# Performance work log

Hardware: AMD Instinct MI355X
Metric: run time of the kernel (lower is better)

## Reference

```python
import jax, jax.numpy as jnp
import numpy as np

B, S, H = 2, 1024, 2048
E, I, K = 32, 768, 4


def setup_inputs() -> dict:
    key = jax.random.key(0)
    k1, k2, k3, k4, k5 = jax.random.split(key, 5)
    sH = 1.0 / np.sqrt(H)
    sI = 1.0 / np.sqrt(I)
    return {
        "hidden_states": jax.random.normal(k1, (B, S, H), dtype=jnp.float32),
        "gate_w": jax.random.normal(k2, (E, H), dtype=jnp.float32) * sH,
        "w_gate": jax.random.normal(k3, (E, H, I), dtype=jnp.float32) * sH,
        "w_up": jax.random.normal(k4, (E, H, I), dtype=jnp.float32) * sH,
        "w_down": jax.random.normal(k5, (E, I, H), dtype=jnp.float32) * sI,
        "top_k": K,
    }


def reference(hidden_states, gate_w, w_gate, w_up, w_down, top_k):
    b, s, h = hidden_states.shape
    x = hidden_states.reshape(-1, h)                      # [T, H]
    T = x.shape[0]

    # Router: logits -> softmax over experts -> top-k -> renormalize
    logits = x @ gate_w.T                                 # [T, E]
    probs = jax.nn.softmax(logits, axis=-1)
    topv, topi = jax.lax.top_k(probs, top_k)              # [T, K]
    topv = topv / jnp.sum(topv, axis=-1, keepdims=True)   # norm_topk_prob

    # Dense routing-weight matrix (zero except selected experts) [T, E]
    rw = jnp.zeros((T, probs.shape[-1]), dtype=x.dtype)
    rw = rw.at[jnp.arange(T)[:, None], topi].set(topv)

    # Expert SwiGLU MLPs, computed for all experts then masked-combined
    g = jnp.einsum('th,ehi->eti', x, w_gate)              # [E, T, I]
    u = jnp.einsum('th,ehi->eti', x, w_up)                # [E, T, I]
    act = jax.nn.silu(g) * u                              # [E, T, I]
    expert_out = jnp.einsum('eti,eih->eth', act, w_down)  # [E, T, H]

    out = jnp.einsum('te,eth->th', rw, expert_out)        # combine [T, H]
    return out.reshape(b, s, h).astype(hidden_states.dtype)
```

## Files before the change

### kernel.cpp

```cpp
#include <hip/hip_runtime.h>
#include <hip/hip_bf16.h>
#include <math.h>

typedef unsigned short u16;
typedef unsigned int u32;
typedef unsigned long long u64;
typedef short s16x8 __attribute__((ext_vector_type(8)));
typedef u16 u16x8 __attribute__((ext_vector_type(8)));
typedef u32 u32x2 __attribute__((ext_vector_type(2)));
typedef u32 u32x4 __attribute__((ext_vector_type(4)));
typedef float f32x4 __attribute__((ext_vector_type(4)));

#define TTOK 2048
#define HDIM 2048
#define ENUM 32
#define IDIM 768
#define KTOP 4

#define WS_XB   0L
#define WS_ACT  8388608L
#define WS_TIDX 20971520L
#define WS_TW   (WS_TIDX + 32768L)
#define WS_CNT  (WS_TW + 32768L)
#define WS_OFFS (WS_CNT + 128L)
#define WS_CUR  (WS_OFFS + 256L)
#define WS_RTOK (WS_CUR + 128L)
#define WS_RW   (WS_RTOK + 32768L)
#define WS_RMAP (WS_RW + 32768L)
#define WS_EO   25165824L
#define WS_NEED (WS_EO + 33554432L)

#define LDBW 20

__device__ __forceinline__ u16 f2bf(float f) {
  unsigned u = __builtin_bit_cast(unsigned, f);
  unsigned r = (u + 0x7fffu + ((u >> 16) & 1u)) >> 16;
  return (u16)r;
}

__device__ __forceinline__ u32 cvtpk(float lo, float hi) {
  u32 r;
  asm("v_cvt_pk_bf16_f32 %0, %1, %2" : "=v"(r) : "v"(lo), "v"(hi));
  return r;
}

__device__ __forceinline__ void gll16(const void* g, void* l) {
  u32 loff = __builtin_amdgcn_readfirstlane((u32)(u64)l);
  __builtin_amdgcn_global_load_lds(
      (const __attribute__((address_space(1))) u32*)(u64)g,
      (__attribute__((address_space(3))) u32*)loff, 16, 0, 0);
}

__device__ __forceinline__ s16x8 bfrag(const u32* B, int d0, int d1) {
  u32x2 lo = *(const u32x2*)(B + d0);
  u32x2 hi = *(const u32x2*)(B + d1);
  u32x4 v = {lo.x, lo.y, hi.x, hi.y};
  return __builtin_bit_cast(s16x8, v);
}

__global__ __launch_bounds__(256) void router_kernel(const float* __restrict__ x,
                                                     const float* __restrict__ gw,
                                                     u16* __restrict__ xb,
                                                     int* __restrict__ tidx,
                                                     float* __restrict__ tw,
                                                     int* __restrict__ counts) {
  __shared__ float xs[HDIM];
  __shared__ float part[256];
  __shared__ float lg[ENUM];
  int t = blockIdx.x;
  const float4* xr = (const float4*)(x + (long)t * HDIM);
  float4* xs4 = (float4*)xs;
  for (int i = threadIdx.x; i < HDIM / 4; i += 256) xs4[i] = xr[i];
  __syncthreads();
  {
    int i0 = threadIdx.x * 8;
    uint4 o;
    o.x = cvtpk(xs[i0], xs[i0 + 1]);
    o.y = cvtpk(xs[i0 + 2], xs[i0 + 3]);
    o.z = cvtpk(xs[i0 + 4], xs[i0 + 5]);
    o.w = cvtpk(xs[i0 + 6], xs[i0 + 7]);
    *(uint4*)(xb + (long)t * HDIM + i0) = o;
  }
  int e = threadIdx.x >> 3, ch = threadIdx.x & 7;
  const float4* gp = (const float4*)(gw + (long)e * HDIM + ch * 256);
  const float4* xp = (const float4*)(xs + ch * 256);
  float s = 0.f;
#pragma unroll 8
  for (int c = 0; c < 64; c++) {
    float4 gv = gp[c], xv = xp[c];
    s += gv.x * xv.x + gv.y * xv.y + gv.z * xv.z + gv.w * xv.w;
  }
  part[threadIdx.x] = s;
  __syncthreads();
  if (threadIdx.x < 32) {
    float v = 0.f;
#pragma unroll
    for (int j = 0; j < 8; j++) v += part[threadIdx.x * 8 + j];
    lg[threadIdx.x] = v;
  }
  __syncthreads();
  if (threadIdx.x == 0) {
    int sel[KTOP]; float sv[KTOP];
    unsigned mask = 0;
    for (int k = 0; k < KTOP; k++) {
      float best = -INFINITY; int bi = 0;
      for (int j = 0; j < ENUM; j++)
        if (!((mask >> j) & 1u) && lg[j] > best) { best = lg[j]; bi = j; }
      mask |= 1u << bi; sel[k] = bi; sv[k] = best;
    }
    float m = sv[0], den = 0.f, ex[KTOP];
    for (int k = 0; k < KTOP; k++) { ex[k] = expf(sv[k] - m); den += ex[k]; }
    for (int k = 0; k < KTOP; k++) {
      tidx[t * KTOP + k] = sel[k];
      tw[t * KTOP + k] = ex[k] / den;
      atomicAdd(&counts[sel[k]], 1);
    }
  }
}

__global__ void scan_kernel(const int* __restrict__ counts, int* __restrict__ offs,
                            int* __restrict__ cur) {
  if (threadIdx.x == 0) {
    int a = 0;
    for (int e = 0; e < ENUM; e++) { offs[e] = a; a += counts[e]; }
    offs[ENUM] = a;
  }
  if (threadIdx.x < ENUM) cur[threadIdx.x] = 0;
}

__global__ __launch_bounds__(256) void scatter_kernel(const int* __restrict__ tidx,
                                                      const float* __restrict__ tw,
                                                      const int* __restrict__ offs,
                                                      int* __restrict__ cur,
                                                      int* __restrict__ rtok,
                                                      float* __restrict__ rw,
                                                      int* __restrict__ rowmap) {
  int i = blockIdx.x * 256 + threadIdx.x;
  int e = tidx[i];
  int pos = atomicAdd(&cur[e], 1);
  int row = offs[e] + pos;
  rtok[row] = i >> 2;
  rw[row] = tw[i];
  rowmap[i] = row;
}

__global__ __launch_bounds__(512) void gemm1_kernel(const u16* __restrict__ xb,
                                                    const float* __restrict__ wgp,
                                                    const float* __restrict__ wup,
                                                    const int* __restrict__ offs,
                                                    const int* __restrict__ rtok,
                                                    u16* __restrict__ act) {
  int d = blockIdx.x;
  int g = d % 384;
  int mt = d / 384;
  int e = g / 12;
  int nt = g % 12;
  int off = offs[e], cnt = offs[e + 1] - off;
  int m0 = mt << 8;
  if (m0 >= cnt) return;
  int rows = cnt - m0; if (rows > 256) rows = 256;
  int baser = off + m0;
  int n0 = nt << 6;

  __shared__ __align__(16) u16 As[2][256 * 32];
  __shared__ __align__(16) u32 Bs[2][2][64 * LDBW];

  int tid = threadIdx.x;
  int ln = tid & 63, w = tid >> 6;
  int wm = w >> 1, wn = w & 1;
  int lhi = ln >> 4, llo = ln & 15;

  const u16* gA[2];
  int ldsA[2];
#pragma unroll
  for (int j = 0; j < 2; j++) {
    int idx = w * 2 + j;
    int r = idx * 16 + (ln >> 2);
    int c = ln & 3;
    int csrc = c ^ ((r >> 1) & 3);
    int rr = r < rows ? r : rows - 1;
    gA[j] = xb + (long)rtok[baser + rr] * HDIM + csrc * 8;
    ldsA[j] = idx * 1024;
  }

  int mat = tid >> 8;
  int t2 = tid & 255;
  int a = t2 & 15;
  int kk = t2 >> 4;
  const float* gB = (mat ? wup : wgp) + (long)e * ((long)HDIM * IDIM) +
                    (long)(2 * kk) * IDIM + n0 + 4 * a;
  int fB = 2 * (a & 7);
  int wOff[4];
#pragma unroll
  for (int j = 0; j < 4; j++) wOff[j] = (4 * a + j) * LDBW + (kk ^ fB);

  int offA[4];
#pragma unroll
  for (int mf = 0; mf < 4; mf++) {
    int r = wm * 64 + mf * 16 + llo;
    offA[mf] = r * 64 + ((lhi ^ ((r >> 1) & 3)) * 16);
  }
  int dB0[2], dB1[2];
#pragma unroll
  for (int nf = 0; nf < 2; nf++) {
    int n = wn * 32 + nf * 16 + llo;
    int f = 2 * ((n >> 2) & 7);
    dB0[nf] = n * LDBW + ((4 * lhi) ^ f);
    dB1[nf] = n * LDBW + (((4 * lhi) | 2) ^ f);
  }

  f32x4 accg[4][2], accu[4][2];
  f32x4 zz = {0.f, 0.f, 0.f, 0.f};
#pragma unroll
  for (int i = 0; i < 4; i++)
#pragma unroll
    for (int j = 0; j < 2; j++) { accg[i][j] = zz; accu[i][j] = zz; }

  float4 rB0, rB1;

  rB0 = *(const float4*)gB;
  rB1 = *(const float4*)(gB + IDIM);
  gll16(gA[0], (char*)As[0] + ldsA[0]);
  gll16(gA[1], (char*)As[0] + ldsA[1]);
  {
    u32* bb = &Bs[0][mat][0];
    bb[wOff[0]] = cvtpk(rB0.x, rB1.x);
    bb[wOff[1]] = cvtpk(rB0.y, rB1.y);
    bb[wOff[2]] = cvtpk(rB0.z, rB1.z);
    bb[wOff[3]] = cvtpk(rB0.w, rB1.w);
  }
  __syncthreads();

  const int NS = HDIM / 32;
  int buf = 0;
  for (int t = 0; t < NS; ++t) {
    if (t + 1 < NS) {
      const float* p = gB + (long)(t + 1) * 32 * IDIM;
      rB0 = *(const float4*)p;
      rB1 = *(const float4*)(p + IDIM);
      gll16(gA[0] + (t + 1) * 32, (char*)As[buf ^ 1] + ldsA[0]);
      gll16(gA[1] + (t + 1) * 32, (char*)As[buf ^ 1] + ldsA[1]);
    }
    __builtin_amdgcn_sched_barrier(0);
    {
      const char* Ab = (const char*)As[buf];
      const u32* Bg = &Bs[buf][0][0];
      const u32* Bu = &Bs[buf][1][0];
      s16x8 av[4];
#pragma unroll
      for (int mf = 0; mf < 4; mf++) av[mf] = *(const s16x8*)(Ab + offA[mf]);
#pragma unroll
      for (int nf = 0; nf < 2; nf++) {
        s16x8 bg = bfrag(Bg, dB0[nf], dB1[nf]);
        s16x8 bu = bfrag(Bu, dB0[nf], dB1[nf]);
#pragma unroll
        for (int mf = 0; mf < 4; mf++) {
          accg[mf][nf] = __builtin_amdgcn_mfma_f32_16x16x32_bf16(av[mf], bg, accg[mf][nf], 0, 0, 0);
          accu[mf][nf] = __builtin_amdgcn_mfma_f32_16x16x32_bf16(av[mf], bu, accu[mf][nf], 0, 0, 0);
        }
      }
    }
    if (t + 1 < NS) {
      u32* bb = &Bs[buf ^ 1][mat][0];
      bb[wOff[0]] = cvtpk(rB0.x, rB1.x);
      bb[wOff[1]] = cvtpk(rB0.y, rB1.y);
      bb[wOff[2]] = cvtpk(rB0.z, rB1.z);
      bb[wOff[3]] = cvtpk(rB0.w, rB1.w);
    }
    __syncthreads();
    buf ^= 1;
  }

  int rb = wm * 64 + lhi * 4;
  int cb = n0 + wn * 32 + llo;
#pragma unroll
  for (int mf = 0; mf < 4; mf++) {
#pragma unroll
    for (int r4 = 0; r4 < 4; r4++) {
      int rl = rb + mf * 16 + r4;
      if (rl < rows) {
        long rowb = (long)(baser + rl) * IDIM;
#pragma unroll
        for (int nf = 0; nf < 2; nf++) {
          float g2 = accg[mf][nf][r4], u = accu[mf][nf][r4];
          float av = g2 / (1.f + __expf(-g2)) * u;
          act[rowb + cb + nf * 16] = f2bf(av);
        }
      }
    }
  }
}

template <int STORE>
__global__ __launch_bounds__(512) void gemm2_kernel(const u16* __restrict__ act,
                                                    const float* __restrict__ wdp,
                                                    const int* __restrict__ offs,
                                                    const int* __restrict__ rtok,
                                                    const float* __restrict__ rw,
                                                    u16* __restrict__ eo,
                                                    float* __restrict__ out) {
  int d = blockIdx.x;
  int g = d & 511;
  int mt = d >> 9;
  int e = g >> 4;
  int nt = g & 15;
  int off = offs[e], cnt = offs[e + 1] - off;
  int m0 = mt << 8;
  if (m0 >= cnt) return;
  int rows = cnt - m0; if (rows > 256) rows = 256;
  int baser = off + m0;
  int n0 = nt << 7;

  __shared__ __align__(16) u16 As[2][256 * 32];
  __shared__ __align__(16) u32 Bs[2][128 * LDBW];

  int tid = threadIdx.x;
  int ln = tid & 63, w = tid >> 6;
  int wm = w >> 1, wn = w & 1;
  int lhi = ln >> 4, llo = ln & 15;

  const u16* gA[2];
  int ldsA[2];
#pragma unroll
  for (int j = 0; j < 2; j++) {
    int idx = w * 2 + j;
    int r = idx * 16 + (ln >> 2);
    int c = ln & 3;
    int csrc = c ^ ((r >> 1) & 3);
    int rr = r < rows ? r : rows - 1;
    gA[j] = act + (long)(baser + rr) * IDIM + csrc * 8;
    ldsA[j] = idx * 1024;
  }

  int a = tid & 31;
  int kk = (tid >> 5) & 15;
  const float* gB = wdp + (long)e * ((long)IDIM * HDIM) +
                    (long)(2 * kk) * HDIM + n0 + 4 * a;
  int fB = 2 * (a & 7);
  int wOff[4];
#pragma unroll
  for (int j = 0; j < 4; j++) wOff[j] = (4 * a + j) * LDBW + (kk ^ fB);

  int offA[4];
#pragma unroll
  for (int mf = 0; mf < 4; mf++) {
    int r = wm * 64 + mf * 16 + llo;
    offA[mf] = r * 64 + ((lhi ^ ((r >> 1) & 3)) * 16);
  }
  int dB0[4], dB1[4];
#pragma unroll
  for (int nf = 0; nf < 4; nf++) {
    int n = wn * 64 + nf * 16 + llo;
    int f = 2 * ((n >> 2) & 7);
    dB0[nf] = n * LDBW + ((4 * lhi) ^ f);
    dB1[nf] = n * LDBW + (((4 * lhi) | 2) ^ f);
  }

  f32x4 acc[4][4];
  f32x4 zz = {0.f, 0.f, 0.f, 0.f};
#pragma unroll
  for (int i = 0; i < 4; i++)
#pragma unroll
    for (int j = 0; j < 4; j++) acc[i][j] = zz;

  float4 rB0, rB1;

  rB0 = *(const float4*)gB;
  rB1 = *(const float4*)(gB + HDIM);
  gll16(gA[0], (char*)As[0] + ldsA[0]);
  gll16(gA[1], (char*)As[0] + ldsA[1]);
  {
    u32* bb = &Bs[0][0];
    bb[wOff[0]] = cvtpk(rB0.x, rB1.x);
    bb[wOff[1]] = cvtpk(rB0.y, rB1.y);
    bb[wOff[2]] = cvtpk(rB0.z, rB1.z);
    bb[wOff[3]] = cvtpk(rB0.w, rB1.w);
  }
  __syncthreads();

  const int NS = IDIM / 32;
  int buf = 0;
  for (int t = 0; t < NS; ++t) {
    if (t + 1 < NS) {
      const float* p = gB + (long)(t + 1) * 32 * HDIM;
      rB0 = *(const float4*)p;
      rB1 = *(const float4*)(p + HDIM);
      gll16(gA[0] + (t + 1) * 32, (char*)As[buf ^ 1] + ldsA[0]);
      gll16(gA[1] + (t + 1) * 32, (char*)As[buf ^ 1] + ldsA[1]);
    }
    __builtin_amdgcn_sched_barrier(0);
    {
      const char* Ab = (const char*)As[buf];
      const u32* Bb = &Bs[buf][0];
      s16x8 av[4];
#pragma unroll
      for (int mf = 0; mf < 4; mf++) av[mf] = *(const s16x8*)(Ab + offA[mf]);
#pragma unroll
      for (int nf = 0; nf < 4; nf++) {
        s16x8 bv = bfrag(Bb, dB0[nf], dB1[nf]);
#pragma unroll
        for (int mf = 0; mf < 4; mf++)
          acc[mf][nf] = __builtin_amdgcn_mfma_f32_16x16x32_bf16(av[mf], bv, acc[mf][nf], 0, 0, 0);
      }
    }
    if (t + 1 < NS) {
      u32* bb = &Bs[buf ^ 1][0];
      bb[wOff[0]] = cvtpk(rB0.x, rB1.x);
      bb[wOff[1]] = cvtpk(rB0.y, rB1.y);
      bb[wOff[2]] = cvtpk(rB0.z, rB1.z);
      bb[wOff[3]] = cvtpk(rB0.w, rB1.w);
    }
    __syncthreads();
    buf ^= 1;
  }

  int rb = wm * 64 + lhi * 4;
  int cb = n0 + wn * 64 + llo;
#pragma unroll
  for (int mf = 0; mf < 4; mf++) {
#pragma unroll
    for (int r4 = 0; r4 < 4; r4++) {
      int rl = rb + mf * 16 + r4;
      if (rl < rows) {
        int rr = baser + rl;
        if (STORE) {
          long ob = (long)rr * HDIM + cb;
#pragma unroll
          for (int nf = 0; nf < 4; nf++)
            eo[ob + nf * 16] = f2bf(acc[mf][nf][r4]);
        } else {
          float wt = rw[rr];
          long ob = (long)rtok[rr] * HDIM + cb;
#pragma unroll
          for (int nf = 0; nf < 4; nf++)
            atomicAdd(&out[ob + nf * 16], acc[mf][nf][r4] * wt);
        }
      }
    }
  }
}

__global__ __launch_bounds__(256) void combine_kernel(const u16* __restrict__ eo,
                                                      const int* __restrict__ rowmap,
                                                      const float* __restrict__ tw,
                                                      float* __restrict__ out) {
  int t = blockIdx.x;
  int h0 = threadIdx.x * 8;
  float acc[8] = {0.f, 0.f, 0.f, 0.f, 0.f, 0.f, 0.f, 0.f};
#pragma unroll
  for (int k = 0; k < KTOP; k++) {
    int r = rowmap[t * KTOP + k];
    float wt = tw[t * KTOP + k];
    u16x8 v = *(const u16x8*)(eo + (long)r * HDIM + h0);
#pragma unroll
    for (int j = 0; j < 8; j++)
      acc[j] += wt * __builtin_bit_cast(float, ((u32)v[j]) << 16);
  }
  float4 o0 = {acc[0], acc[1], acc[2], acc[3]};
  float4 o1 = {acc[4], acc[5], acc[6], acc[7]};
  *(float4*)(out + (long)t * HDIM + h0) = o0;
  *(float4*)(out + (long)t * HDIM + h0 + 4) = o1;
}

extern "C" void kernel_launch(void* const* d_in, const int* in_sizes, int n_in,
                              void* d_out, int out_size, void* d_ws, size_t ws_size,
                              hipStream_t stream) {
  const float* x = (const float*)d_in[0];
  const float* gw = (const float*)d_in[1];
  const float* wgate = (const float*)d_in[2];
  const float* wup = (const float*)d_in[3];
  const float* wdown = (const float*)d_in[4];
  float* out = (float*)d_out;

  char* ws = (char*)d_ws;
  u16* xb = (u16*)(ws + WS_XB);
  u16* act = (u16*)(ws + WS_ACT);
  int* tidx = (int*)(ws + WS_TIDX);
  float* tw = (float*)(ws + WS_TW);
  int* cnt = (int*)(ws + WS_CNT);
  int* offs = (int*)(ws + WS_OFFS);
  int* cur = (int*)(ws + WS_CUR);
  int* rtok = (int*)(ws + WS_RTOK);
  float* rw = (float*)(ws + WS_RW);
  int* rowmap = (int*)(ws + WS_RMAP);
  u16* eo = (u16*)(ws + WS_EO);
  bool storeMode = (ws_size >= (size_t)WS_NEED);

  hipMemsetAsync(cnt, 0, 128, stream);
  if (!storeMode)
    hipMemsetAsync(d_out, 0, (size_t)out_size * sizeof(float), stream);

  hipLaunchKernelGGL(router_kernel, dim3(TTOK), dim3(256), 0, stream, x, gw, xb, tidx, tw, cnt);
  hipLaunchKernelGGL(scan_kernel, dim3(1), dim3(64), 0, stream, cnt, offs, cur);
  hipLaunchKernelGGL(scatter_kernel, dim3(TTOK * KTOP / 256), dim3(256), 0, stream, tidx, tw, offs, cur, rtok, rw, rowmap);
  hipLaunchKernelGGL(gemm1_kernel, dim3(32 * 12 * 8), dim3(512), 0, stream, xb, wgate, wup, offs, rtok, act);
  if (storeMode) {
    hipLaunchKernelGGL(gemm2_kernel<1>, dim3(32 * 16 * 8), dim3(512), 0, stream, act, wdown, offs, rtok, rw, eo, out);
    hipLaunchKernelGGL(combine_kernel, dim3(TTOK), dim3(256), 0, stream, eo, rowmap, tw, out);
  } else {
    hipLaunchKernelGGL(gemm2_kernel<0>, dim3(32 * 16 * 8), dim3(512), 0, stream, act, wdown, offs, rtok, rw, eo, out);
  }
}
```

Baseline: 370.2 us.

## Split gate/up GEMM into separate tiles and add a SwiGLU fuse kernel

In store mode the fused gate+up GEMM is replaced by a kernel where each block computes only one of the two matrices for its tile. This doubles the grid and halves the B-tile shared memory per block. Gate and up results go to bf16 scratch buffers, and a separate elementwise kernel applies SiLU(g)*u to build the activation. The aim is more parallelism and occupancy, at the cost of reading A twice, extra global traffic for the intermediates, an extra launch, and bf16 rounding of g and u before the activation.

```diff
diff --git a/kernel.cpp b/kernel.cpp
--- a/kernel.cpp
+++ b/kernel.cpp
@@ -28,6 +28,8 @@
 #define WS_RW   (WS_RTOK + 32768L)
 #define WS_RMAP (WS_RW + 32768L)
 #define WS_EO   25165824L
+#define WS_GBUF WS_EO
+#define WS_UBUF (WS_EO + 12582912L)
 #define WS_NEED (WS_EO + 33554432L)
 
 #define LDBW 20
@@ -144,12 +146,175 @@
   rowmap[i] = row;
 }
 
-__global__ __launch_bounds__(512) void gemm1_kernel(const u16* __restrict__ xb,
-                                                    const float* __restrict__ wgp,
-                                                    const float* __restrict__ wup,
-                                                    const int* __restrict__ offs,
-                                                    const int* __restrict__ rtok,
-                                                    u16* __restrict__ act) {
+__global__ __launch_bounds__(512) void gemm1s_kernel(const u16* __restrict__ xb,
+                                                     const float* __restrict__ wgp,
+                                                     const float* __restrict__ wup,
+                                                     const int* __restrict__ offs,
+                                                     const int* __restrict__ rtok,
+                                                     u16* __restrict__ gbuf,
+                                                     u16* __restrict__ ubuf) {
+  int d = blockIdx.x;
+  int g = d % 768;
+  int mt = d / 768;
+  int e = g / 24;
+  int r24 = g % 24;
+  int nt = r24 >> 1;
+  int mat = r24 & 1;
+  int off = offs[e], cnt = offs[e + 1] - off;
+  int m0 = mt << 8;
+  if (m0 >= cnt) return;
+  int rows = cnt - m0; if (rows > 256) rows = 256;
+  int baser = off + m0;
+  int n0 = nt << 6;
+
+  __shared__ __align__(16) u16 As[2][256 * 32];
+  __shared__ __align__(16) u32 Bs[2][64 * LDBW];
+
+  int tid = threadIdx.x;
+  int ln = tid & 63, w = tid >> 6;
+  int wm = w >> 1, wn = w & 1;
+  int lhi = ln >> 4, llo = ln & 15;
+
+  const u16* gA[2];
+  int ldsA[2];
+#pragma unroll
+  for (int j = 0; j < 2; j++) {
+    int idx = w * 2 + j;
+    int r = idx * 16 + (ln >> 2);
+    int c = ln & 3;
+    int csrc = c ^ ((r >> 1) & 3);
+    int rr = r < rows ? r : rows - 1;
+    gA[j] = xb + (long)rtok[baser + rr] * HDIM + csrc * 8;
+    ldsA[j] = idx * 1024;
+  }
+
+  int isB = (tid < 256);
+  int a = tid & 15;
+  int kk = (tid >> 4) & 15;
+  const float* gB = (mat ? wup : wgp) + (long)e * ((long)HDIM * IDIM) +
+                    (long)(2 * kk) * IDIM + n0 + 4 * a;
+  int fB = 2 * (a & 7);
+  int wOff[4];
+#pragma unroll
+  for (int j = 0; j < 4; j++) wOff[j] = (4 * a + j) * LDBW + (kk ^ fB);
+
+  int offA[4];
+#pragma unroll
+  for (int mf = 0; mf < 4; mf++) {
+    int r = wm * 64 + mf * 16 + llo;
+    offA[mf] = r * 64 + ((lhi ^ ((r >> 1) & 3)) * 16);
+  }
+  int dB0[2], dB1[2];
+#pragma unroll
+  for (int nf = 0; nf < 2; nf++) {
+    int n = wn * 32 + nf * 16 + llo;
+    int f = 2 * ((n >> 2) & 7);
+    dB0[nf] = n * LDBW + ((4 * lhi) ^ f);
+    dB1[nf] = n * LDBW + (((4 * lhi) | 2) ^ f);
+  }
+
+  f32x4 acc[4][2];
+  f32x4 zz = {0.f, 0.f, 0.f, 0.f};
+#pragma unroll
+  for (int i = 0; i < 4; i++)
+#pragma unroll
+    for (int j = 0; j < 2; j++) acc[i][j] = zz;
+
+  float4 rB0, rB1;
+
+  if (isB) {
+    rB0 = *(const float4*)gB;
+    rB1 = *(const float4*)(gB + IDIM);
+  }
+  gll16(gA[0], (char*)As[0] + ldsA[0]);
+  gll16(gA[1], (char*)As[0] + ldsA[1]);
+  if (isB) {
+    u32* bb = &Bs[0][0];
+    bb[wOff[0]] = cvtpk(rB0.x, rB1.x);
+    bb[wOff[1]] = cvtpk(rB0.y, rB1.y);
+    bb[wOff[2]] = cvtpk(rB0.z, rB1.z);
+    bb[wOff[3]] = cvtpk(rB0.w, rB1.w);
+  }
+  __syncthreads();
+
+  const int NS = HDIM / 32;
+  int buf = 0;
+  for (int t = 0; t < NS; ++t) {
+    if (t + 1 < NS) {
+      if (isB) {
+        const float* p = gB + (long)(t + 1) * 32 * IDIM;
+        rB0 = *(const float4*)p;
+        rB1 = *(const float4*)(p + IDIM);
+      }
+      gll16(gA[0] + (t + 1) * 32, (char*)As[buf ^ 1] + ldsA[0]);
+      gll16(gA[1] + (t + 1) * 32, (char*)As[buf ^ 1] + ldsA[1]);
+    }
+    __builtin_amdgcn_sched_barrier(0);
+    {
+      const char* Ab = (const char*)As[buf];
+      const u32* Bb = &Bs[buf][0];
+      s16x8 av[4];
+#pragma unroll
+      for (int mf = 0; mf < 4; mf++) av[mf] = *(const s16x8*)(Ab + offA[mf]);
+#pragma unroll
+      for (int nf = 0; nf < 2; nf++) {
+        s16x8 bv = bfrag(Bb, dB0[nf], dB1[nf]);
+#pragma unroll
+        for (int mf = 0; mf < 4; mf++)
+          acc[mf][nf] = __builtin_amdgcn_mfma_f32_16x16x32_bf16(av[mf], bv, acc[mf][nf], 0, 0, 0);
+      }
+    }
+    if (t + 1 < NS && isB) {
+      u32* bb = &Bs[buf ^ 1][0];
+      bb[wOff[0]] = cvtpk(rB0.x, rB1.x);
+      bb[wOff[1]] = cvtpk(rB0.y, rB1.y);
+      bb[wOff[2]] = cvtpk(rB0.z, rB1.z);
+      bb[wOff[3]] = cvtpk(rB0.w, rB1.w);
+    }
+    __syncthreads();
+    buf ^= 1;
+  }
+
+  u16* ob = mat ? ubuf : gbuf;
+  int rb = wm * 64 + lhi * 4;
+  int cb = n0 + wn * 32 + llo;
+#pragma unroll
+  for (int mf = 0; mf < 4; mf++) {
+#pragma unroll
+    for (int r4 = 0; r4 < 4; r4++) {
+      int rl = rb + mf * 16 + r4;
+      if (rl < rows) {
+        long rowb = (long)(baser + rl) * IDIM;
+#pragma unroll
+        for (int nf = 0; nf < 2; nf++)
+          ob[rowb + cb + nf * 16] = f2bf(acc[mf][nf][r4]);
+      }
+    }
+  }
+}
+
+__global__ __launch_bounds__(256) void fuse_kernel(const u16* __restrict__ gbuf,
+                                                   const u16* __restrict__ ubuf,
+                                                   u16* __restrict__ act) {
+  long i = ((long)blockIdx.x * 256 + threadIdx.x) * 8;
+  u16x8 gv = *(const u16x8*)(gbuf + i);
+  u16x8 uv = *(const u16x8*)(ubuf + i);
+  u16x8 o;
+#pragma unroll
+  for (int j = 0; j < 8; j++) {
+    float g = __builtin_bit_cast(float, ((u32)gv[j]) << 16);
+    float u = __builtin_bit_cast(float, ((u32)uv[j]) << 16);
+    o[j] = f2bf(g / (1.f + __expf(-g)) * u);
+  }
+  *(u16x8*)(act + i) = o;
+}
+
+__global__ __launch_bounds__(512) void gemm1f_kernel(const u16* __restrict__ xb,
+                                                     const float* __restrict__ wgp,
+                                                     const float* __restrict__ wup,
+                                                     const int* __restrict__ offs,
+                                                     const int* __restrict__ rtok,
+                                                     u16* __restrict__ act) {
   int d = blockIdx.x;
   int g = d % 384;
   int mt = d / 384;
@@ -483,6 +648,8 @@
   int* rtok = (int*)(ws + WS_RTOK);
   float* rw = (float*)(ws + WS_RW);
   int* rowmap = (int*)(ws + WS_RMAP);
+  u16* gbuf = (u16*)(ws + WS_GBUF);
+  u16* ubuf = (u16*)(ws + WS_UBUF);
   u16* eo = (u16*)(ws + WS_EO);
   bool storeMode = (ws_size >= (size_t)WS_NEED);
 
@@ -493,11 +660,13 @@
   hipLaunchKernelGGL(router_kernel, dim3(TTOK), dim3(256), 0, stream, x, gw, xb, tidx, tw, cnt);
   hipLaunchKernelGGL(scan_kernel, dim3(1), dim3(64), 0, stream, cnt, offs, cur);
   hipLaunchKernelGGL(scatter_kernel, dim3(TTOK * KTOP / 256), dim3(256), 0, stream, tidx, tw, offs, cur, rtok, rw, rowmap);
-  hipLaunchKernelGGL(gemm1_kernel, dim3(32 * 12 * 8), dim3(512), 0, stream, xb, wgate, wup, offs, rtok, act);
   if (storeMode) {
+    hipLaunchKernelGGL(gemm1s_kernel, dim3(768 * 8), dim3(512), 0, stream, xb, wgate, wup, offs, rtok, gbuf, ubuf);
+    hipLaunchKernelGGL(fuse_kernel, dim3(TTOK * KTOP * IDIM / (256 * 8)), dim3(256), 0, stream, gbuf, ubuf, act);
     hipLaunchKernelGGL(gemm2_kernel<1>, dim3(32 * 16 * 8), dim3(512), 0, stream, act, wdown, offs, rtok, rw, eo, out);
     hipLaunchKernelGGL(combine_kernel, dim3(TTOK), dim3(256), 0, stream, eo, rowmap, tw, out);
   } else {
+    hipLaunchKernelGGL(gemm1f_kernel, dim3(32 * 12 * 8), dim3(512), 0, stream, xb, wgate, wup, offs, rtok, act);
     hipLaunchKernelGGL(gemm2_kernel<0>, dim3(32 * 16 * 8), dim3(512), 0, stream, act, wdown, offs, rtok, rw, eo, out);
   }
 }
```

Result: slower. 409.2 us (+10.5%).
